# Optimization experiments

Measured on AMD Instinct MI355X. Metric: run time of the kernel, lower is better.

## Reference

```python
import jax, jax.numpy as jnp
import numpy as np

NEG_INF = -1.0e9  # matches torch masked_fill value


def setup_inputs() -> dict:
    key = jax.random.key(0)
    k1, k2 = jax.random.split(key)
    bs, seq_len, emb_dim = 8, 4096, 512
    max_num_patches = 1024
    h = jax.random.normal(k1, (bs, seq_len, emb_dim), dtype=jnp.float32)
    patch_ids = jnp.sort(
        jax.random.randint(k2, (bs, seq_len), 0, max_num_patches), axis=-1
    )
    return {"h": h, "patch_ids": patch_ids,
            "max_num_patches": max_num_patches, "k": 2}


def reference(h, patch_ids, max_num_patches, k):
    """topk_mean pooling: for each patch (segment) and embedding dim, average
    the top-k values of h among tokens belonging to that patch. Patches with
    fewer than k tokens average only the available tokens; empty patches -> 0.
    Faithful to the torch scatter_reduce(amax)+mask loop."""
    bs, seq_len, emb_dim = h.shape
    b_idx = jnp.arange(bs)[:, None]  # [bs,1] broadcast with patch_ids [bs,seq]
    # tokens-per-patch counts (equivalent of one_hot.sum(dim=1))
    counts = jnp.zeros((bs, max_num_patches), h.dtype).at[b_idx, patch_ids].add(1.0)

    h_work = h
    collected = []
    for _ in range(k):  # k is a small static constant (default 2)
        # segmented amax over tokens -> [bs, P, E]; empty patches get 0
        # (torch scatter_reduce with include_self=False on a zeros base)
        scattered = (jnp.full((bs, max_num_patches, emb_dim), -jnp.inf, h.dtype)
                     .at[b_idx, patch_ids].max(h_work))
        current_max = jnp.where(counts[:, :, None] > 0, scattered, jnp.zeros((), h.dtype))
        collected.append(current_max)
        # gather per-token patch max and mask out positions equal to it
        cur_exp = current_max[b_idx, patch_ids]  # [bs, seq, E]
        h_work = jnp.where(h_work == cur_exp, jnp.asarray(NEG_INF, h.dtype), h_work)

    topk_vals = jnp.stack(collected, axis=2)  # [bs, P, k, E]
    valid = (jnp.arange(k)[None, None, :] < counts[:, :, None]).astype(h.dtype)  # [bs,P,k]
    sum_valid = (topk_vals * valid[..., None]).sum(axis=2)          # [bs, P, E]
    num_valid = jnp.clip(valid.sum(axis=2), 1.0, None)              # [bs, P]
    return sum_valid / num_valid[..., None]
```

## Files before the change

### kernel.cpp

```cpp
#include <hip/hip_runtime.h>


#define NEG_INF (-1.0e9f)
#define D 8

typedef float vf4 __attribute__((ext_vector_type(4)));

__global__ __launch_bounds__(128) void topk_mean_pool_fused(
    const float* __restrict__ h,
    const int*   __restrict__ pid,
    const int*   __restrict__ d_P,
    const int*   __restrict__ d_k,
    float*       __restrict__ out,
    int bs_seq, int pairs, int E)
{
    const int P   = *d_P;
    const int bs  = pairs / P;
    const int seq = bs_seq / bs;
    const int kk  = *d_k;

    const int pair = blockIdx.x;
    const int b    = pair / P;
    const int p    = pair - b * P;

    __shared__ int sb[2];
    if (threadIdx.x < 2) {
        const int  tgt = p + (int)threadIdx.x;
        const int* row = pid + (size_t)b * seq;
        int lo = 0, hi = seq;
        while (lo < hi) {
            const int mid = (lo + hi) >> 1;
            if (row[mid] < tgt) lo = mid + 1; else hi = mid;
        }
        sb[threadIdx.x] = lo;
    }
    __syncthreads();

    const int start = sb[0];
    const int end   = sb[1];
    const int n     = end - start;

    const int Ed4 = E >> 2;
    const vf4* hb   = reinterpret_cast<const vf4*>(h) + (size_t)b * seq * Ed4;
    vf4*       out4 = reinterpret_cast<vf4*>(out) + (size_t)pair * Ed4;

    for (int c = threadIdx.x; c < Ed4; c += blockDim.x) {
        vf4 r;
        if (n == 0) {
            r = (vf4){0.f, 0.f, 0.f, 0.f};
        } else {
            vf4 m1 = (vf4){-INFINITY, -INFINITY, -INFINITY, -INFINITY};
            vf4 m2 = m1;
            int t = start;
            while (t < end) {
                const int nload = min(D, end - t);
                vf4 v[D];
#pragma unroll
                for (int d = 0; d < D; ++d)
                    if (d < nload)
                        v[d] = __builtin_nontemporal_load(
                                   &hb[(size_t)(t + d) * Ed4 + c]);
#pragma unroll
                for (int d = 0; d < D; ++d) {
                    if (d < nload) {
                        const vf4 vv = v[d];
                        if (vv.x > m1.x) { m2.x = m1.x; m1.x = vv.x; }
                        else if (vv.x < m1.x && vv.x > m2.x) { m2.x = vv.x; }
                        if (vv.y > m1.y) { m2.y = m1.y; m1.y = vv.y; }
                        else if (vv.y < m1.y && vv.y > m2.y) { m2.y = vv.y; }
                        if (vv.z > m1.z) { m2.z = m1.z; m1.z = vv.z; }
                        else if (vv.z < m1.z && vv.z > m2.z) { m2.z = vv.z; }
                        if (vv.w > m1.w) { m2.w = m1.w; m1.w = vv.w; }
                        else if (vv.w < m1.w && vv.w > m2.w) { m2.w = vv.w; }
                    }
                }
                t += nload;
            }
            if (n == 1 || kk == 1) {
                r = m1;
            } else {
                r.x = 0.5f * (m1.x + fmaxf(m2.x, NEG_INF));
                r.y = 0.5f * (m1.y + fmaxf(m2.y, NEG_INF));
                r.z = 0.5f * (m1.z + fmaxf(m2.z, NEG_INF));
                r.w = 0.5f * (m1.w + fmaxf(m2.w, NEG_INF));
            }
        }
        __builtin_nontemporal_store(r, &out4[c]);
    }
}

extern "C" void kernel_launch(void* const* d_in, const int* in_sizes, int n_in,
                              void* d_out, int out_size, void* d_ws, size_t ws_size,
                              hipStream_t stream) {
    const float* h   = (const float*)d_in[0];
    const int*   pid = (const int*)d_in[1];
    const int*   d_P = (const int*)d_in[2];
    const int*   d_k = (const int*)d_in[3];
    float*       out = (float*)d_out;
    (void)d_ws; (void)ws_size; (void)n_in;

    const int h_elems = in_sizes[0];
    const int bs_seq  = in_sizes[1];
    const int E       = h_elems / bs_seq;
    const int pairs   = out_size / E;

    dim3 grid(pairs), block(128);
    topk_mean_pool_fused<<<grid, block, 0, stream>>>(h, pid, d_P, d_k, out,
                                                     bs_seq, pairs, E);
}
```

Before: 118.9 us.

## Find patch bounds via shared-memory window scan instead of binary search

```diff
diff --git a/kernel.cpp b/kernel.cpp
--- a/kernel.cpp
+++ b/kernel.cpp
@@ -3,10 +3,9 @@
 
 #define NEG_INF (-1.0e9f)
 #define D 8
+#define W 256
 
-typedef float vf4 __attribute__((ext_vector_type(4)));
-
-__global__ __launch_bounds__(128) void topk_mean_pool_fused(
+__global__ __launch_bounds__(128) void topk_mean_pool_win(
     const float* __restrict__ h,
     const int*   __restrict__ pid,
     const int*   __restrict__ d_P,
@@ -23,14 +22,46 @@
     const int b    = pair / P;
     const int p    = pair - b * P;
 
+    __shared__ int swin[W + 1];
     __shared__ int sb[2];
-    if (threadIdx.x < 2) {
-        const int  tgt = p + (int)threadIdx.x;
-        const int* row = pid + (size_t)b * seq;
+
+    const int* row = pid + (size_t)b * seq;
+
+    int w0 = (int)(((long long)seq * p) / P) - W / 2;
+    if (w0 < 0) w0 = 0;
+    if (w0 > seq - W) w0 = seq - W;
+    if (w0 < 0) w0 = 0;
+
+    if (threadIdx.x < 2) sb[threadIdx.x] = -1;
+    {
+        const int i0 = threadIdx.x, i1 = threadIdx.x + 128;
+        const int g0 = w0 + i0, g1 = w0 + i1;
+        swin[i0] = (g0 < seq) ? row[g0] : 0x7fffffff;
+        swin[i1] = (g1 < seq) ? row[g1] : 0x7fffffff;
+        if (threadIdx.x == 0) {
+            const int g2 = w0 + W;
+            swin[W] = (g2 < seq) ? row[g2] : 0x7fffffff;
+        }
+    }
+    __syncthreads();
+
+#pragma unroll
+    for (int x = 0; x < 2; ++x) {
+        const int t  = p + x;
+        const int i0 = threadIdx.x + 1;
+        const int i1 = threadIdx.x + 129;
+        if (swin[i0 - 1] < t && swin[i0] >= t) sb[x] = w0 + i0;
+        if (swin[i1 - 1] < t && swin[i1] >= t) sb[x] = w0 + i1;
+        if (threadIdx.x == 0 && w0 == 0 && swin[0] >= t) sb[x] = 0;
+    }
+    __syncthreads();
+
+    if (threadIdx.x < 2 && sb[threadIdx.x] < 0) {
+        const int t = p + (int)threadIdx.x;
         int lo = 0, hi = seq;
         while (lo < hi) {
             const int mid = (lo + hi) >> 1;
-            if (row[mid] < tgt) lo = mid + 1; else hi = mid;
+            if (row[mid] < t) lo = mid + 1; else hi = mid;
         }
         sb[threadIdx.x] = lo;
     }
@@ -41,29 +72,27 @@
     const int n     = end - start;
 
     const int Ed4 = E >> 2;
-    const vf4* hb   = reinterpret_cast<const vf4*>(h) + (size_t)b * seq * Ed4;
-    vf4*       out4 = reinterpret_cast<vf4*>(out) + (size_t)pair * Ed4;
+    const float4* hb   = (const float4*)h + (size_t)b * seq * Ed4;
+    float4*       out4 = (float4*)out + (size_t)pair * Ed4;
 
     for (int c = threadIdx.x; c < Ed4; c += blockDim.x) {
-        vf4 r;
+        float4 r;
         if (n == 0) {
-            r = (vf4){0.f, 0.f, 0.f, 0.f};
+            r = make_float4(0.f, 0.f, 0.f, 0.f);
         } else {
-            vf4 m1 = (vf4){-INFINITY, -INFINITY, -INFINITY, -INFINITY};
-            vf4 m2 = m1;
+            float4 m1 = make_float4(-INFINITY, -INFINITY, -INFINITY, -INFINITY);
+            float4 m2 = m1;
             int t = start;
             while (t < end) {
                 const int nload = min(D, end - t);
-                vf4 v[D];
+                float4 v[D];
 #pragma unroll
                 for (int d = 0; d < D; ++d)
-                    if (d < nload)
-                        v[d] = __builtin_nontemporal_load(
-                                   &hb[(size_t)(t + d) * Ed4 + c]);
+                    if (d < nload) v[d] = hb[(size_t)(t + d) * Ed4 + c];
 #pragma unroll
                 for (int d = 0; d < D; ++d) {
                     if (d < nload) {
-                        const vf4 vv = v[d];
+                        const float4 vv = v[d];
                         if (vv.x > m1.x) { m2.x = m1.x; m1.x = vv.x; }
                         else if (vv.x < m1.x && vv.x > m2.x) { m2.x = vv.x; }
                         if (vv.y > m1.y) { m2.y = m1.y; m1.y = vv.y; }
@@ -85,7 +114,7 @@
                 r.w = 0.5f * (m1.w + fmaxf(m2.w, NEG_INF));
             }
         }
-        __builtin_nontemporal_store(r, &out4[c]);
+        out4[c] = r;
     }
 }
 
@@ -105,6 +134,6 @@
     const int pairs   = out_size / E;
 
     dim3 grid(pairs), block(128);
-    topk_mean_pool_fused<<<grid, block, 0, stream>>>(h, pid, d_P, d_k, out,
-                                                     bs_seq, pairs, E);
+    topk_mean_pool_win<<<grid, block, 0, stream>>>(h, pid, d_P, d_k, out,
+                                                   bs_seq, pairs, E);
 }
```

Measured after the change: 106.5 us (median of 2 runs). 10.5% less time.
